# Kernel optimization log

Hardware: AMD Instinct MI355X
Metric: run time of the kernel (lower is better)

The kernel has to match this reference:

```python
import jax, jax.numpy as jnp
import numpy as np

K, PMAX, NUM_PTS = 20000, 30, 5
GEO_DIM, PE_DIM = 256, 32
C_OUT = GEO_DIM - PE_DIM  # 224
NUM_FREQS = 8


def setup_inputs() -> dict:
    key = jax.random.key(0)
    k = jax.random.split(key, 6)
    geoms = jax.random.normal(k[0], (K, PMAX, 2), dtype=jnp.float32) * 8.0  # ego BEV meters
    lengths = jax.random.randint(k[1], (K,), 2, PMAX + 1)                   # valid points per polyline
    w1 = jax.random.normal(k[2], (C_OUT // 2, 2, 3), jnp.float32) * 0.2
    b1 = jax.random.normal(k[3], (C_OUT // 2,), jnp.float32) * 0.02
    w2 = jax.random.normal(k[4], (C_OUT, C_OUT // 2, 3), jnp.float32) * 0.05
    b2 = jax.random.normal(k[5], (C_OUT,), jnp.float32) * 0.02
    gamma = jnp.ones((C_OUT,), jnp.float32)
    beta = jnp.zeros((C_OUT,), jnp.float32)
    return {"geoms": geoms, "lengths": lengths, "w1": w1, "b1": b1,
            "w2": w2, "b2": b2, "gamma": gamma, "beta": beta,
            "roi_w": 60, "roi_h": 30}


def _resample_one(coords, L):
    # coords: [PMAX,2] padded polyline; L: scalar int (>=2 valid points)
    diffs = coords[1:] - coords[:-1]                                  # [PMAX-1,2]
    sq = jnp.sum(diffs * diffs, axis=1)
    mask = (jnp.arange(PMAX - 1) < (L - 1)).astype(coords.dtype)      # valid segments
    seg = jnp.where(sq > 0, jnp.sqrt(jnp.where(sq > 0, sq, 1.0)), 0.0) * mask
    cum = jnp.concatenate([jnp.zeros((1,), coords.dtype), jnp.cumsum(seg)])  # [PMAX]
    total = cum[-1]
    targets = jnp.linspace(0.0, 1.0, NUM_PTS, dtype=coords.dtype) * total
    idx = jnp.clip(jnp.searchsorted(cum, targets, side='left'), 1, L - 1)
    t = (targets - cum[idx - 1]) / (seg[idx - 1] + 1e-8)
    pts = coords[idx - 1] + t[:, None] * diffs[idx - 1]               # [NUM_PTS,2]
    degen = total < 1e-6
    return jnp.where(degen, jnp.broadcast_to(coords[0], pts.shape), pts)


def _conv1d(x, w, b):
    # x: [K,C,5]; w: [O,C,3]; 'same' padding 1
    y = jax.lax.conv_general_dilated(x, w, (1,), ((1, 1),),
                                     dimension_numbers=('NCH', 'OIH', 'NCH'))
    return y + b[None, :, None]


def reference(geoms, lengths, w1, b1, w2, b2, gamma, beta, roi_w, roi_h):
    resampled = jax.vmap(_resample_one)(geoms, lengths)               # [K,5,2]
    roi_half = jnp.array([roi_w / 2.0, roi_h / 2.0], jnp.float32)
    roi_full = jnp.array([float(roi_w), float(roi_h)], jnp.float32)
    coords = (resampled + roi_half) / roi_full                        # [K,5,2] in [0,1]
    # sinusoidal PE: per coord dim [sin(x*2^f*pi) x8 | cos x8] -> flatten to 32
    freqs = (2.0 ** jnp.arange(NUM_FREQS, dtype=jnp.float32)) * np.float32(np.pi)
    xf = coords[..., None] * freqs                                    # [K,5,2,8]
    pe = jnp.concatenate([jnp.sin(xf), jnp.cos(xf)], axis=-1).reshape(-1, NUM_PTS, PE_DIM)
    x = coords.transpose(0, 2, 1)                                     # [K,2,5]
    x = jax.nn.relu(_conv1d(x, w1, b1))                               # [K,112,5]
    x = jax.nn.relu(_conv1d(x, w2, b2))                               # [K,224,5]
    x = x.transpose(0, 2, 1)                                          # [K,5,224]
    mu = jnp.mean(x, axis=-1, keepdims=True)
    var = jnp.mean((x - mu) ** 2, axis=-1, keepdims=True)
    x = (x - mu) * jax.lax.rsqrt(var + 1e-5) * gamma + beta
    geo_feats = jnp.concatenate([pe, x], axis=-1)                     # [K,5,256]
    return geo_feats, coords
```

## Files before the change

### kernel.cpp

```cpp
#include <hip/hip_runtime.h>
#include <math.h>

#define K_POLY   20000
#define PMAX     30
#define NUM_PTS  5
#define C_MID    112
#define C_OUT    224
#define PE_DIM   32
#define GEO_DIM  256
#define M_ROWS   (K_POLY*NUM_PTS)

#define NTILES   14
#define KSTEPS   11
#define WP_ELEMS (KSTEPS*NTILES*64*8)
#define NPACK_BLK ((WP_ELEMS+255)/256)

#define GROUP_US 8192

#define ROWS_W   32
#define NUNITS   (M_ROWS/ROWS_W)
#define NPREP_BLK NUNITS
#define WAVES2_B 8
#define NBLK2    256
#define TOTW2    (NBLK2*WAVES2_B)

typedef __attribute__((ext_vector_type(8))) short short8;
typedef __attribute__((ext_vector_type(4))) float f32x4;

__device__ inline unsigned short f2bf(float f) {
    union { float f; unsigned u; } v; v.f = f;
    return (unsigned short)((v.u + 0x7fffu + ((v.u >> 16) & 1u)) >> 16);
}

#define GLDS(gp, lp) __builtin_amdgcn_global_load_lds( \
    (const __attribute__((address_space(1))) void*)(gp), \
    (__attribute__((address_space(3))) void*)(lp), 16, 0, 0)

#define SH_PITCH 120

__global__ __launch_bounds__(256) void prep_pack(
    const float* __restrict__ geoms, const int* __restrict__ lengths,
    const float* __restrict__ w1, const float* __restrict__ b1,
    const float* __restrict__ w2,
    const int* __restrict__ roi_w, const int* __restrict__ roi_h,
    unsigned short* __restrict__ Wp, float* __restrict__ out)
{
    __shared__ unsigned short s_h[40 * SH_PITCH];

    if (blockIdx.x < NPACK_BLK) {
        int i = blockIdx.x * 256 + threadIdx.x;
        if (i < WP_ELEMS) {
            int j    = i & 7;
            int lane = (i >> 3) & 63;
            int grp  = i >> 9;
            int nt   = grp % NTILES;
            int ks   = grp / NTILES;
            int k    = ks * 32 + (lane >> 4) * 8 + j;
            int n    = nt * 16 + (lane & 15);
            float v = 0.f;
            if (k < 336) {
                int dk = k / C_MID, c = k - dk * C_MID;
                v = w2[(n * C_MID + c) * 3 + dk];
            }
            Wp[i] = f2bf(v);
        }
        return;
    }

    const int ub     = blockIdx.x - NPACK_BLK;
    const int rbase0 = ub * ROWS_W;
    const int pstart = rbase0 / 5;
    const int npoly  = (rbase0 + 31) / 5 - pstart + 1;

    const int t = threadIdx.x, lane = t & 63, wave = t >> 6;
    const float roiw  = (float)roi_w[0], roih = (float)roi_h[0];
    const float halfx = roiw * 0.5f, halfy = roih * 0.5f;

    for (int lp = wave; lp < 8; lp += 4) {
        if (lp < npoly) {
            const int poly = pstart + lp;
            const float* gp = geoms + (size_t)poly * (PMAX * 2);
            float px = 0.f, py = 0.f;
            if (lane < PMAX) { float2 p = ((const float2*)gp)[lane]; px = p.x; py = p.y; }
            const int L = lengths[poly];

            float nx = __shfl(px, lane + 1);
            float ny = __shfl(py, lane + 1);
            float seg = 0.f;
            if (lane < L - 1 && lane < PMAX - 1) {
                float dx = nx - px, dy = ny - py;
                float sq = dx * dx + dy * dy;
                seg = (sq > 0.f) ? sqrtf(sq) : 0.f;
            }
            float incl = seg;
            #pragma unroll
            for (int d = 1; d < 32; d <<= 1) {
                float v = __shfl_up(incl, d, 32);
                if ((lane & 31) >= d) incl += v;
            }
            float cum = __shfl_up(incl, 1, 32);
            if ((lane & 31) == 0) cum = 0.f;
            const float total = __shfl(incl, PMAX - 2);
            const bool degen = total < 1e-6f;
            const float x0g = __shfl(px, 0), y0g = __shfl(py, 0);

            float bxv[NUM_PTS], byv[NUM_PTS];
            #pragma unroll
            for (int j = 0; j < NUM_PTS; ++j) {
                float tj = total * (0.25f * (float)j);
                unsigned long long mlt = __ballot(lane < PMAX && cum < tj);
                int idx = (int)__popcll(mlt);
                idx = max(1, min(idx, L - 1));
                float c1 = __shfl(cum, idx - 1);
                float s1 = __shfl(seg, idx - 1);
                float ax = __shfl(px, idx - 1), ay = __shfl(py, idx - 1);
                float bx2 = __shfl(px, idx),    by2 = __shfl(py, idx);
                float tt = (tj - c1) / (s1 + 1e-8f);
                float fx = degen ? x0g : ax + tt * (bx2 - ax);
                float fy = degen ? y0g : ay + tt * (by2 - ay);
                bxv[j] = (fx + halfx) / roiw;
                byv[j] = (fy + halfy) / roih;
            }
            if (lane == 0) {
                float* co = out + (size_t)M_ROWS * GEO_DIM + (size_t)poly * (NUM_PTS * 2);
                #pragma unroll
                for (int j = 0; j < NUM_PTS; ++j) { co[2 * j] = bxv[j]; co[2 * j + 1] = byv[j]; }
            }

            #pragma unroll
            for (int it = 0; it < 2; ++it) {
                int c = it * 64 + lane;
                if (c < C_MID) {
                    const float* w = w1 + c * 6;
                    float w0 = w[0], wa = w[1], wb = w[2], w3 = w[3], w4 = w[4], w5 = w[5];
                    float bb = b1[c];
                    #pragma unroll
                    for (int pp = 0; pp < NUM_PTS; ++pp) {
                        float acc = bb + bxv[pp] * wa + byv[pp] * w4;
                        if (pp > 0)           acc += bxv[pp - 1] * w0 + byv[pp - 1] * w3;
                        if (pp < NUM_PTS - 1) acc += bxv[pp + 1] * wb + byv[pp + 1] * w5;
                        s_h[(lp * 5 + pp) * SH_PITCH + c] = f2bf(fmaxf(acc, 0.f));
                    }
                }
            }
        }
    }
    __syncthreads();

    unsigned short* Af = (unsigned short*)out;
    for (int cidx = t; cidx < 2 * KSTEPS * 64; cidx += 256) {
        int gl  = cidx / (KSTEPS * 64);
        int rem = cidx - gl * (KSTEPS * 64);
        int ks  = rem >> 6;
        int ln  = rem & 63;
        int q   = ln >> 4, rr = ln & 15;
        int r   = (2 * ub + gl) * 16 + rr;
        int p   = r % 5;
        int lp5 = (r - pstart * 5) - p;

        union { short8 v; unsigned long long u2[2]; } val;
        val.u2[0] = 0ull; val.u2[1] = 0ull;
        int k0 = ks * 32 + q * 8;
        if (k0 < 336) {
            int dk = k0 / C_MID;
            int c0 = k0 - dk * C_MID;
            int pp = p + dk - 1;
            if (pp >= 0 && pp < NUM_PTS)
                val.v = *(const short8*)&s_h[(lp5 + pp) * SH_PITCH + c0];
        }
        *(short8*)(Af + (size_t)(2 * ub + gl) * GROUP_US + ks * 512 + ln * 8) = val.v;
    }
}

__global__ __launch_bounds__(512, 2) void gemm2(
    const unsigned short* __restrict__ Wp,
    const float* __restrict__ b2, const float* __restrict__ gamma,
    const float* __restrict__ beta, float* __restrict__ out)
{
    __shared__ __align__(16) unsigned short s_B[WP_ELEMS];

    const int t = threadIdx.x, lane = t & 63, wave = t >> 6;
    const int quad = lane >> 4, m = lane & 15;

    #pragma unroll
    for (int it = 0; it < 20; ++it) {
        int idx = t + it * 512;
        if (idx < WP_ELEMS / 8)
            GLDS((const char*)Wp + (size_t)idx * 16, (char*)s_B + idx * 16);
    }
    __syncthreads();

    const unsigned short* Af = (const unsigned short*)out;
    const float* cptr = out + (size_t)M_ROWS * GEO_DIM;
    const unsigned short* bl = s_B + lane * 8;

    for (int u = blockIdx.x * WAVES2_B + wave; u < NUNITS; u += TOTW2) {
        const int rw = u * ROWS_W;

        const unsigned short* Ab0 = Af + (size_t)(2 * u) * GROUP_US + lane * 8;
        const unsigned short* Ab1 = Ab0 + GROUP_US;

        float cv = cptr[(size_t)rw * 2 + lane];

        f32x4 acc0[NTILES], acc1[NTILES];
        #pragma unroll
        for (int nt = 0; nt < NTILES; ++nt)
            #pragma unroll
            for (int i = 0; i < 4; ++i) { acc0[nt][i] = 0.f; acc1[nt][i] = 0.f; }

        short8 a0 = *(const short8*)Ab0;
        short8 a1 = *(const short8*)Ab1;
        #pragma unroll
        for (int ks = 0; ks < KSTEPS; ++ks) {
            short8 a0n = a0, a1n = a1;
            if (ks < KSTEPS - 1) {
                a0n = *(const short8*)(Ab0 + (ks + 1) * 512);
                a1n = *(const short8*)(Ab1 + (ks + 1) * 512);
            }
            const unsigned short* bp = bl + ks * (NTILES * 512);
            __builtin_amdgcn_s_setprio(1);
            #pragma unroll
            for (int nt = 0; nt < NTILES; ++nt) {
                short8 b = *(const short8*)(bp + nt * 512);
                acc0[nt] = __builtin_amdgcn_mfma_f32_16x16x32_bf16(a0, b, acc0[nt], 0, 0, 0);
                acc1[nt] = __builtin_amdgcn_mfma_f32_16x16x32_bf16(a1, b, acc1[nt], 0, 0, 0);
            }
            __builtin_amdgcn_s_setprio(0);
            a0 = a0n; a1 = a1n;
        }

        {
            const int col = lane & 31;
            const int d = col >> 4, isc = (col >> 3) & 1, fr = col & 7;
            const float pef = (float)(1 << fr) * 3.14159265358979323846f;
            #pragma unroll
            for (int it = 0; it < 16; ++it) {
                int j2 = it * 2 + (lane >> 5);
                float x = __shfl(cv, j2 * 2 + d);
                float arg = x * pef;
                out[(size_t)(rw + j2) * GEO_DIM + col] = isc ? __cosf(arg) : __sinf(arg);
            }
        }

        float bias[NTILES], gm[NTILES], bt[NTILES];
        #pragma unroll
        for (int nt = 0; nt < NTILES; ++nt) {
            int col = nt * 16 + m;
            bias[nt] = b2[col]; gm[nt] = gamma[col]; bt[nt] = beta[col];
        }

        #pragma unroll
        for (int g = 0; g < 2; ++g) {
            f32x4* acc = g ? acc1 : acc0;
            #pragma unroll
            for (int i = 0; i < 4; ++i) {
                float s = 0.f, q = 0.f;
                #pragma unroll
                for (int nt = 0; nt < NTILES; ++nt) {
                    float v = fmaxf(acc[nt][i] + bias[nt], 0.f);
                    acc[nt][i] = v;
                    s += v; q += v * v;
                }
                #pragma unroll
                for (int mk = 8; mk >= 1; mk >>= 1) {
                    s += __shfl_xor(s, mk, 64);
                    q += __shfl_xor(q, mk, 64);
                }
                float mu  = s * (1.f / C_OUT);
                float var = fmaxf(q * (1.f / C_OUT) - mu * mu, 0.f);
                float rs  = rsqrtf(var + 1e-5f);
                int r = rw + g * 16 + quad * 4 + i;
                size_t ob = (size_t)r * GEO_DIM + PE_DIM + m;
                #pragma unroll
                for (int nt = 0; nt < NTILES; ++nt)
                    out[ob + nt * 16] = (acc[nt][i] - mu) * rs * gm[nt] + bt[nt];
            }
        }
    }
}

extern "C" void kernel_launch(void* const* d_in, const int* in_sizes, int n_in,
                              void* d_out, int out_size, void* d_ws, size_t ws_size,
                              hipStream_t stream) {
    const float* geoms   = (const float*)d_in[0];
    const int*   lengths = (const int*)d_in[1];
    const float* w1      = (const float*)d_in[2];
    const float* b1      = (const float*)d_in[3];
    const float* w2      = (const float*)d_in[4];
    const float* b2      = (const float*)d_in[5];
    const float* gamma   = (const float*)d_in[6];
    const float* beta    = (const float*)d_in[7];
    const int*   roi_w   = (const int*)d_in[8];
    const int*   roi_h   = (const int*)d_in[9];
    float* out = (float*)d_out;
    unsigned short* Wp = (unsigned short*)d_ws;

    hipLaunchKernelGGL(prep_pack, dim3(NPACK_BLK + NPREP_BLK), dim3(256), 0, stream,
                       geoms, lengths, w1, b1, w2, roi_w, roi_h, Wp, out);
    hipLaunchKernelGGL(gemm2, dim3(NBLK2), dim3(512), 0, stream, Wp, b2, gamma, beta, out);
}
```

Baseline: 175.8 us.

## Halve per-wave row tile in gemm2 and double waves per block

Result: slower. 511.1 us (+190.7%).

```diff
diff --git a/kernel.cpp b/kernel.cpp
--- a/kernel.cpp
+++ b/kernel.cpp
@@ -20,7 +20,9 @@
 #define ROWS_W   32
 #define NUNITS   (M_ROWS/ROWS_W)
 #define NPREP_BLK NUNITS
-#define WAVES2_B 8
+
+#define NGROUPS  (M_ROWS/16)
+#define WAVES2_B 16
 #define NBLK2    256
 #define TOTW2    (NBLK2*WAVES2_B)
 
@@ -172,7 +174,7 @@
     }
 }
 
-__global__ __launch_bounds__(512, 2) void gemm2(
+__global__ __launch_bounds__(1024, 4) void gemm2(
     const unsigned short* __restrict__ Wp,
     const float* __restrict__ b2, const float* __restrict__ gamma,
     const float* __restrict__ beta, float* __restrict__ out)
@@ -183,8 +185,8 @@
     const int quad = lane >> 4, m = lane & 15;
 
     #pragma unroll
-    for (int it = 0; it < 20; ++it) {
-        int idx = t + it * 512;
+    for (int it = 0; it < 10; ++it) {
+        int idx = t + it * 1024;
         if (idx < WP_ELEMS / 8)
             GLDS((const char*)Wp + (size_t)idx * 16, (char*)s_B + idx * 16);
     }
@@ -194,39 +196,34 @@
     const float* cptr = out + (size_t)M_ROWS * GEO_DIM;
     const unsigned short* bl = s_B + lane * 8;
 
-    for (int u = blockIdx.x * WAVES2_B + wave; u < NUNITS; u += TOTW2) {
-        const int rw = u * ROWS_W;
-
-        const unsigned short* Ab0 = Af + (size_t)(2 * u) * GROUP_US + lane * 8;
-        const unsigned short* Ab1 = Ab0 + GROUP_US;
-
-        float cv = cptr[(size_t)rw * 2 + lane];
-
-        f32x4 acc0[NTILES], acc1[NTILES];
+    for (int g = blockIdx.x * WAVES2_B + wave; g < NGROUPS; g += TOTW2) {
+        const int rw = g * 16;
+
+        const unsigned short* Ab0 = Af + (size_t)g * GROUP_US + lane * 8;
+
+        float cv = (lane < 32) ? cptr[(size_t)rw * 2 + lane] : 0.f;
+
+        f32x4 acc[NTILES];
         #pragma unroll
         for (int nt = 0; nt < NTILES; ++nt)
             #pragma unroll
-            for (int i = 0; i < 4; ++i) { acc0[nt][i] = 0.f; acc1[nt][i] = 0.f; }
+            for (int i = 0; i < 4; ++i) acc[nt][i] = 0.f;
 
         short8 a0 = *(const short8*)Ab0;
-        short8 a1 = *(const short8*)Ab1;
         #pragma unroll
         for (int ks = 0; ks < KSTEPS; ++ks) {
-            short8 a0n = a0, a1n = a1;
-            if (ks < KSTEPS - 1) {
+            short8 a0n = a0;
+            if (ks < KSTEPS - 1)
                 a0n = *(const short8*)(Ab0 + (ks + 1) * 512);
-                a1n = *(const short8*)(Ab1 + (ks + 1) * 512);
-            }
             const unsigned short* bp = bl + ks * (NTILES * 512);
             __builtin_amdgcn_s_setprio(1);
             #pragma unroll
             for (int nt = 0; nt < NTILES; ++nt) {
                 short8 b = *(const short8*)(bp + nt * 512);
-                acc0[nt] = __builtin_amdgcn_mfma_f32_16x16x32_bf16(a0, b, acc0[nt], 0, 0, 0);
-                acc1[nt] = __builtin_amdgcn_mfma_f32_16x16x32_bf16(a1, b, acc1[nt], 0, 0, 0);
+                acc[nt] = __builtin_amdgcn_mfma_f32_16x16x32_bf16(a0, b, acc[nt], 0, 0, 0);
             }
             __builtin_amdgcn_s_setprio(0);
-            a0 = a0n; a1 = a1n;
+            a0 = a0n;
         }
 
         {
@@ -234,7 +231,7 @@
             const int d = col >> 4, isc = (col >> 3) & 1, fr = col & 7;
             const float pef = (float)(1 << fr) * 3.14159265358979323846f;
             #pragma unroll
-            for (int it = 0; it < 16; ++it) {
+            for (int it = 0; it < 8; ++it) {
                 int j2 = it * 2 + (lane >> 5);
                 float x = __shfl(cv, j2 * 2 + d);
                 float arg = x * pef;
@@ -250,31 +247,27 @@
         }
 
         #pragma unroll
-        for (int g = 0; g < 2; ++g) {
-            f32x4* acc = g ? acc1 : acc0;
-            #pragma unroll
-            for (int i = 0; i < 4; ++i) {
-                float s = 0.f, q = 0.f;
-                #pragma unroll
-                for (int nt = 0; nt < NTILES; ++nt) {
-                    float v = fmaxf(acc[nt][i] + bias[nt], 0.f);
-                    acc[nt][i] = v;
-                    s += v; q += v * v;
-                }
-                #pragma unroll
-                for (int mk = 8; mk >= 1; mk >>= 1) {
-                    s += __shfl_xor(s, mk, 64);
-                    q += __shfl_xor(q, mk, 64);
-                }
-                float mu  = s * (1.f / C_OUT);
-                float var = fmaxf(q * (1.f / C_OUT) - mu * mu, 0.f);
-                float rs  = rsqrtf(var + 1e-5f);
-                int r = rw + g * 16 + quad * 4 + i;
-                size_t ob = (size_t)r * GEO_DIM + PE_DIM + m;
-                #pragma unroll
-                for (int nt = 0; nt < NTILES; ++nt)
-                    out[ob + nt * 16] = (acc[nt][i] - mu) * rs * gm[nt] + bt[nt];
-            }
+        for (int i = 0; i < 4; ++i) {
+            float s = 0.f, q = 0.f;
+            #pragma unroll
+            for (int nt = 0; nt < NTILES; ++nt) {
+                float v = fmaxf(acc[nt][i] + bias[nt], 0.f);
+                acc[nt][i] = v;
+                s += v; q += v * v;
+            }
+            #pragma unroll
+            for (int mk = 8; mk >= 1; mk >>= 1) {
+                s += __shfl_xor(s, mk, 64);
+                q += __shfl_xor(q, mk, 64);
+            }
+            float mu  = s * (1.f / C_OUT);
+            float var = fmaxf(q * (1.f / C_OUT) - mu * mu, 0.f);
+            float rs  = rsqrtf(var + 1e-5f);
+            int r = rw + quad * 4 + i;
+            size_t ob = (size_t)r * GEO_DIM + PE_DIM + m;
+            #pragma unroll
+            for (int nt = 0; nt < NTILES; ++nt)
+                out[ob + nt * 16] = (acc[nt][i] - mu) * rs * gm[nt] + bt[nt];
         }
     }
 }
@@ -297,5 +290,5 @@
 
     hipLaunchKernelGGL(prep_pack, dim3(NPACK_BLK + NPREP_BLK), dim3(256), 0, stream,
                        geoms, lengths, w1, b1, w2, roi_w, roi_h, Wp, out);
-    hipLaunchKernelGGL(gemm2, dim3(NBLK2), dim3(512), 0, stream, Wp, b2, gamma, beta, out);
-}
+    hipLaunchKernelGGL(gemm2, dim3(NBLK2), dim3(1024), 0, stream, Wp, b2, gamma, beta, out);
+}
```
